# Performance work log

Measured on AMD Instinct MI355X. Metric: run time of the kernel, lower is better.

The kernel has to match this reference:

```python
import jax, jax.numpy as jnp
import numpy as np

B, HF, WF, C, A = 8, 32, 32, 1024, 9
N = B * HF * WF * A
IMG = 1024.0
K = 512                 # fixed candidate cap (replaces dynamic tf.where shape)
NUM_CLASSES = 80
FRCNN_FEAT = 256
ALIGN, SAMPLES = 7, 2
DET_THR, NMS_IOU = 0.7, 0.7
BN_EPS = 1e-3


def setup_inputs() -> dict:
    key = jax.random.key(0)
    ks = jax.random.split(key, 8)
    rpn_predictions = jax.random.normal(ks[0], (N,), jnp.float32)

    def rand_boxes(k):
        k1, k2, k3, k4 = jax.random.split(k, 4)
        cy = jax.random.uniform(k1, (N,), minval=0.0, maxval=IMG)
        cx = jax.random.uniform(k2, (N,), minval=0.0, maxval=IMG)
        h = jax.random.uniform(k3, (N,), minval=32.0, maxval=256.0)
        w = jax.random.uniform(k4, (N,), minval=32.0, maxval=256.0)
        return cy, cx, h, w

    cy, cx, h, w = rand_boxes(ks[1])
    rpn_anchors = jnp.stack([cy, cx, h, w], -1)  # center-point format [y,x,h,w]
    cy2, cx2, h2, w2 = rand_boxes(ks[2])
    rpn_rois = jnp.stack([
        jnp.clip(cy2 - h2 / 2, 0, IMG), jnp.clip(cx2 - w2 / 2, 0, IMG),
        jnp.clip(cy2 + h2 / 2, 0, IMG), jnp.clip(cx2 + w2 / 2, 0, IMG)], -1)
    rpn_assignments = jnp.repeat(jnp.arange(B, dtype=jnp.int32), HF * WF * A)
    images_features = jax.random.normal(ks[3], (B, HF, WF, C), jnp.float32)
    W1 = jax.random.normal(ks[4], (C, FRCNN_FEAT), jnp.float32) * 0.02
    b1 = jnp.zeros((FRCNN_FEAT,), jnp.float32)
    gamma = jnp.ones((FRCNN_FEAT,), jnp.float32)
    beta = jnp.zeros((FRCNN_FEAT,), jnp.float32)
    moving_mean = jnp.zeros((FRCNN_FEAT,), jnp.float32)
    moving_var = jnp.ones((FRCNN_FEAT,), jnp.float32)
    W2 = jax.random.normal(ks[5], (FRCNN_FEAT, 4 + NUM_CLASSES), jnp.float32) * 0.02
    b2 = jnp.zeros((4 + NUM_CLASSES,), jnp.float32)
    return dict(rpn_predictions=rpn_predictions, rpn_rois=rpn_rois,
                rpn_anchors=rpn_anchors, rpn_assignments=rpn_assignments,
                images_features=images_features, W1=W1, b1=b1, gamma=gamma,
                beta=beta, moving_mean=moving_mean, moving_var=moving_var,
                W2=W2, b2=b2)


def center_to_corners(a):
    y, x, h, w = a[:, 0], a[:, 1], a[:, 2], a[:, 3]
    return jnp.stack([y - h / 2, x - w / 2, y + h / 2, x + w / 2], -1)


def iou_one(box, boxes):
    yA = jnp.maximum(box[0], boxes[:, 0]); xA = jnp.maximum(box[1], boxes[:, 1])
    yB = jnp.minimum(box[2], boxes[:, 2]); xB = jnp.minimum(box[3], boxes[:, 3])
    inter = jnp.maximum(yB - yA, 0.0) * jnp.maximum(xB - xA, 0.0)
    a1 = (box[2] - box[0]) * (box[3] - box[1])
    a2 = (boxes[:, 2] - boxes[:, 0]) * (boxes[:, 3] - boxes[:, 1])
    return inter / (a1 + a2 - inter + 1e-8)


def greedy_nms(boxes, valid, thr):
    # boxes are already in score-descending order
    k = boxes.shape[0]
    idxs = jnp.arange(k)
    def body(i, keep):
        sup = (iou_one(boxes[i], boxes) > thr) & (idxs > i) & keep[i]
        return keep & ~sup
    return jax.lax.fori_loop(0, k, body, valid)


def roi_align_mean(feats, rois_n, assign):
    # feats [B,H,W,C]; rois_n [K,4] normalized corners; assign [K] batch idx
    Bf, H, W, Cf = feats.shape
    Kc = rois_n.shape[0]
    y1 = rois_n[:, 0] * H; x1 = rois_n[:, 1] * W
    y2 = rois_n[:, 2] * H; x2 = rois_n[:, 3] * W
    S = ALIGN * SAMPLES  # 14 samples per axis
    frac = (jnp.arange(S, dtype=feats.dtype) + 0.5) / S
    ys = y1[:, None] + frac * (y2 - y1)[:, None] - 0.5  # [K,S]
    xs = x1[:, None] + frac * (x2 - x1)[:, None] - 0.5
    yy = jnp.broadcast_to(ys[:, :, None], (Kc, S, S)).reshape(Kc, S * S)
    xx = jnp.broadcast_to(xs[:, None, :], (Kc, S, S)).reshape(Kc, S * S)
    yc = jnp.clip(yy, 0.0, H - 1.0); xc = jnp.clip(xx, 0.0, W - 1.0)
    y0 = jnp.floor(yc); x0 = jnp.floor(xc)
    wy = yc - y0; wx = xc - x0
    y0i = y0.astype(jnp.int32); x0i = x0.astype(jnp.int32)
    y1i = jnp.minimum(y0i + 1, H - 1); x1i = jnp.minimum(x0i + 1, W - 1)
    flat = feats.reshape(Bf * H * W, Cf)
    base = (assign.astype(jnp.int32) * H * W)[:, None]
    def g(yi, xi):
        return flat[(base + yi * W + xi).reshape(-1)].reshape(Kc, S * S, Cf)
    val = (((1 - wy) * (1 - wx))[..., None] * g(y0i, x0i)
           + ((1 - wy) * wx)[..., None] * g(y0i, x1i)
           + (wy * (1 - wx))[..., None] * g(y1i, x0i)
           + (wy * wx)[..., None] * g(y1i, x1i))
    # mean over all samples == mean over the 7x7 bins of per-bin sample means
    return val.mean(axis=1)  # [K,C]


def reference(rpn_predictions, rpn_rois, rpn_anchors, rpn_assignments,
              images_features, W1, b1, gamma, beta, moving_mean, moving_var,
              W2, b2):
    boxes_norm = jnp.array([IMG, IMG, IMG, IMG], jnp.float32)
    # --- threshold + gather (fixed-K top-k replaces dynamic tf.where) ---
    masked = jnp.where(rpn_predictions > DET_THR, rpn_predictions, -jnp.inf)
    top_scores, idx = jax.lax.top_k(masked, K)
    valid = jnp.isfinite(top_scores)
    rois = rpn_rois[idx]
    anchors = rpn_anchors[idx]
    assign = rpn_assignments[idx]
    # --- shift anchors per-image so NMS runs jointly across the batch ---
    shifted = center_to_corners(anchors) + assign[:, None].astype(jnp.float32) * boxes_norm
    # sigmoid is monotone -> score-descending order already holds
    keep = greedy_nms(shifted, valid, NMS_IOU)
    # --- ROI align + head (computed on all K, masked by keep) ---
    pooled = roi_align_mean(images_features, rois / boxes_norm, assign)  # [K,C]
    hdd = pooled @ W1 + b1
    hdd = (hdd - moving_mean) * jax.lax.rsqrt(moving_var + BN_EPS) * gamma + beta
    hdd = jax.nn.relu(hdd)  # dropout inactive at inference
    out = hdd @ W2 + b2  # [K, 4+num_classes]
    keepf = keep.astype(out.dtype)[:, None]
    frcnn_rois = (rois + out[:, :4]) * keepf
    frcnn_predictions = out[:, 4:] * keepf
    return frcnn_predictions, frcnn_rois, keep
```

## Files before the change

### kernel.cpp

```cpp
#include <hip/hip_runtime.h>
#include <stdint.h>

#define NTOT   73728
#define KSEL   512
#define DET_THRf 0.7f
#define NMS_THRf 0.7f
#define HFD    32
#define WFD    32
#define CCH    1024
#define IMGF   1024.0f
#define SAMP   14
#define FEAT1  256
#define OUTD   84
#define MAXC   4096
#define BUCKETS 256
#define BSCALE 48.0f
#define RB     4

#define WS_HIST     0
#define WS_CUTB     1024
#define WS_COUNTER  1028
#define WS_VALID    1032
#define WS_SELIDX   3080
#define WS_CSCORE   5136
#define WS_CIDX     21520
#define WS_ROIS     37904
#define WS_BOXES    46096
#define WS_ASSIGN   54288
#define WS_KEEPF    56336
#define WS_SUP      58384
#define WS_POOLED   91152

__device__ __forceinline__ int bucket_of(float s) {
  int b = (int)((s - DET_THRf) * BSCALE);
  return min(max(b, 0), BUCKETS - 1);
}

__global__ void k_hist(const float* __restrict__ pred, int* __restrict__ hist) {
  __shared__ int lh[BUCKETS];
  int t = threadIdx.x;
  lh[t] = 0;
  __syncthreads();
  for (int i = blockIdx.x * blockDim.x + t; i < NTOT; i += gridDim.x * blockDim.x) {
    float s = pred[i];
    if (s > DET_THRf) atomicAdd(&lh[bucket_of(s)], 1);
  }
  __syncthreads();
  if (lh[t]) atomicAdd(&hist[t], lh[t]);
}

__global__ void k_scan(const int* __restrict__ hist, int* __restrict__ cutB) {
  __shared__ int sh[BUCKETS];
  __shared__ int best;
  int t = threadIdx.x;
  sh[t] = hist[t];
  if (t == 0) best = -1;
  __syncthreads();
  for (int off = 1; off < BUCKETS; off <<= 1) {
    int v = sh[t] + ((t + off < BUCKETS) ? sh[t + off] : 0);
    __syncthreads();
    sh[t] = v;
    __syncthreads();
  }
  if (sh[t] >= KSEL) atomicMax(&best, t);
  __syncthreads();
  if (t == 0) *cutB = (best < 0) ? 0 : best;
}

__global__ void k_collect(const float* __restrict__ pred, const int* __restrict__ cutB,
                          int* __restrict__ counter, float* __restrict__ cs,
                          int* __restrict__ ci) {
  int B = *cutB;
  for (int i = blockIdx.x * blockDim.x + threadIdx.x; i < NTOT; i += gridDim.x * blockDim.x) {
    float s = pred[i];
    if (s > DET_THRf && bucket_of(s) >= B) {
      int p = atomicAdd(counter, 1);
      if (p < MAXC) { cs[p] = s; ci[p] = i; }
    }
  }
}

__global__ void __launch_bounds__(256) k_rank(
    const int* __restrict__ counter, const float* __restrict__ cs, const int* __restrict__ ci,
    int* __restrict__ sel_idx, int* __restrict__ valid) {
  __shared__ float s_s[MAXC];
  __shared__ int   s_i[MAXC];
  int t = threadIdx.x;
  int M = *counter; if (M > MAXC) M = MAXC;
  for (int j = t; j < M; j += 256) { s_s[j] = cs[j]; s_i[j] = ci[j]; }
  __syncthreads();
  int j = blockIdx.x * 256 + t;
  if (j >= M) return;
  float sj = s_s[j]; int ij = s_i[j];
  int r = 0;
  for (int m = 0; m < M; ++m) {
    float sm = s_s[m];
    r += (sm > sj) || (sm == sj && s_i[m] < ij);
  }
  if (r < KSEL) { sel_idx[r] = ij; valid[r] = 1; }
}

__global__ void k_gather(const int* __restrict__ sel_idx, const int* __restrict__ valid,
                         const float* __restrict__ rois, const float* __restrict__ anchors,
                         const int* __restrict__ assign,
                         int* __restrict__ assign_sel, float4* __restrict__ rois_sel,
                         float4* __restrict__ boxes_sh) {
  int t = threadIdx.x;
  if (t >= KSEL) return;
  int v = valid[t];
  int gi = v ? sel_idx[t] : 0;
  float4 rr = make_float4(0.f, 0.f, 0.f, 0.f);
  float4 bx = make_float4(0.f, 0.f, 0.f, 0.f);
  int aa = 0;
  if (v) {
    rr = make_float4(rois[gi*4+0], rois[gi*4+1], rois[gi*4+2], rois[gi*4+3]);
    float cy = anchors[gi*4+0], cx = anchors[gi*4+1];
    float h  = anchors[gi*4+2], w  = anchors[gi*4+3];
    aa = assign[gi];
    float off = (float)aa * IMGF;
    bx = make_float4(cy - h*0.5f + off, cx - w*0.5f + off,
                     cy + h*0.5f + off, cx + w*0.5f + off);
  }
  rois_sel[t] = rr;
  boxes_sh[t] = bx;
  assign_sel[t] = aa;
}

__global__ void k_ioumat(const float4* __restrict__ boxes,
                         unsigned long long* __restrict__ sup) {
  int wave = (blockIdx.x * blockDim.x + threadIdx.x) >> 6;
  int lane = threadIdx.x & 63;
  if (wave >= KSEL) return;
  float4 bi = boxes[wave];
  float a1 = (bi.z - bi.x) * (bi.w - bi.y);
  for (int c = 0; c < 8; ++c) {
    int col = c * 64 + lane;
    float4 bj = boxes[col];
    float yA = fmaxf(bi.x, bj.x), xA = fmaxf(bi.y, bj.y);
    float yB = fminf(bi.z, bj.z), xB = fminf(bi.w, bj.w);
    float inter = fmaxf(yB - yA, 0.f) * fmaxf(xB - xA, 0.f);
    float a2 = (bj.z - bj.x) * (bj.w - bj.y);
    float iou = inter / (a1 + a2 - inter + 1e-8f);
    bool s = (iou > NMS_THRf) && (col > wave);
    unsigned long long m = __ballot(s);
    if (lane == 0) sup[wave * 8 + c] = m;
  }
}

__global__ void k_sweep(const unsigned long long* __restrict__ sup,
                        const int* __restrict__ valid,
                        float* __restrict__ keep_ws, float* __restrict__ keep_out) {
  __shared__ unsigned char kb[KSEL];
  int t = threadIdx.x;
  for (int j = t; j < KSEL; j += 64) kb[j] = (unsigned char)valid[j];
  unsigned long long nz[8];
  for (int w = 0; w < 8; ++w) {
    int row = w * 64 + t;
    const unsigned long long* rp = &sup[row * 8];
    unsigned long long any = rp[0]|rp[1]|rp[2]|rp[3]|rp[4]|rp[5]|rp[6]|rp[7];
    nz[w] = __ballot(any != 0ull);
  }
  __syncthreads();
  if (t == 0) {
    for (int w = 0; w < 8; ++w) {
      unsigned long long bits = nz[w];
      while (bits) {
        int b = __ffsll((unsigned long long)bits) - 1;
        bits &= bits - 1;
        int i = w * 64 + b;
        if (kb[i]) {
          const unsigned long long* rp = &sup[i * 8];
          for (int c = 0; c < 8; ++c) {
            unsigned long long m = rp[c];
            while (m) {
              int bb = __ffsll((unsigned long long)m) - 1;
              m &= m - 1;
              kb[c * 64 + bb] = 0;
            }
          }
        }
      }
    }
  }
  __syncthreads();
  for (int j = t; j < KSEL; j += 64) {
    float kf = kb[j] ? 1.0f : 0.0f;
    keep_ws[j] = kf;
    keep_out[j] = kf;
  }
}

__global__ void __launch_bounds__(256) k_pool(
    const float* __restrict__ feats,
    const float4* __restrict__ rois_sel, const int* __restrict__ assign_sel,
    float* __restrict__ pooled) {
  int r = blockIdx.x;
  int t = threadIdx.x;

  __shared__ float Wy[HFD], Wx[WFD];
  __shared__ int bnds[4];
  __shared__ float wcomb[128];
  __shared__ int   ocomb[128];

  if (t < 32) { Wy[t] = 0.f; Wx[t] = 0.f; }
  __syncthreads();
  if (t == 0) {
    float4 roi = rois_sel[r];
    float sc = (float)HFD / IMGF;
    float y1 = roi.x * sc, x1 = roi.y * sc, y2 = roi.z * sc, x2 = roi.w * sc;
    int ymin = HFD - 1, ymax = 0, xmin = WFD - 1, xmax = 0;
    for (int s = 0; s < SAMP; ++s) {
      float fr = ((float)s + 0.5f) / (float)SAMP;
      float yc = y1 + fr * (y2 - y1) - 0.5f;
      yc = fminf(fmaxf(yc, 0.0f), (float)(HFD - 1));
      float y0f = floorf(yc);
      int y0 = (int)y0f;
      int y1i = min(y0 + 1, HFD - 1);
      float wy = yc - y0f;
      Wy[y0] += 1.0f - wy;
      Wy[y1i] += wy;
      ymin = min(ymin, y0); ymax = max(ymax, y1i);

      float xc = x1 + fr * (x2 - x1) - 0.5f;
      xc = fminf(fmaxf(xc, 0.0f), (float)(WFD - 1));
      float x0f = floorf(xc);
      int x0 = (int)x0f;
      int x1i = min(x0 + 1, WFD - 1);
      float wx = xc - x0f;
      Wx[x0] += 1.0f - wx;
      Wx[x1i] += wx;
      xmin = min(xmin, x0); xmax = max(xmax, x1i);
    }
    bnds[0] = ymin; bnds[1] = ymax; bnds[2] = xmin; bnds[3] = xmax;
  }
  __syncthreads();

  int ymin = bnds[0], xmin = bnds[2];
  int spanY = bnds[1] - ymin + 1;
  int spanX = bnds[3] - xmin + 1;
  int np = spanY * spanX;
  int b = assign_sel[r];
  const float inv = 1.0f / (float)(SAMP * SAMP);

  int ty = t >> 4, tx = t & 15;
  if (ty < spanY && tx < spanX) {
    int p = ty * spanX + tx;
    int y = ymin + ty, x = xmin + tx;
    wcomb[p] = Wy[y] * Wx[x] * inv;
    ocomb[p] = ((b * HFD + y) * WFD + x) * (CCH / 4);
  }
  __syncthreads();

  const float4* f4 = (const float4*)feats;
  float4 a0 = make_float4(0.f,0.f,0.f,0.f), a1 = a0, a2 = a0, a3 = a0;
  int p = 0;
  for (; p + 4 <= np; p += 4) {
    float w0 = wcomb[p],   w1 = wcomb[p+1], w2 = wcomb[p+2], w3 = wcomb[p+3];
    int   o0 = ocomb[p],   o1 = ocomb[p+1], o2 = ocomb[p+2], o3 = ocomb[p+3];
    float4 v0 = f4[o0 + t], v1 = f4[o1 + t], v2 = f4[o2 + t], v3 = f4[o3 + t];
    a0.x += w0*v0.x; a0.y += w0*v0.y; a0.z += w0*v0.z; a0.w += w0*v0.w;
    a1.x += w1*v1.x; a1.y += w1*v1.y; a1.z += w1*v1.z; a1.w += w1*v1.w;
    a2.x += w2*v2.x; a2.y += w2*v2.y; a2.z += w2*v2.z; a2.w += w2*v2.w;
    a3.x += w3*v3.x; a3.y += w3*v3.y; a3.z += w3*v3.z; a3.w += w3*v3.w;
  }
  for (; p < np; ++p) {
    float w = wcomb[p];
    float4 v = f4[ocomb[p] + t];
    a0.x += w*v.x; a0.y += w*v.y; a0.z += w*v.z; a0.w += w*v.w;
  }
  float4 s;
  s.x = (a0.x + a1.x) + (a2.x + a3.x);
  s.y = (a0.y + a1.y) + (a2.y + a3.y);
  s.z = (a0.z + a1.z) + (a2.z + a3.z);
  s.w = (a0.w + a1.w) + (a2.w + a3.w);
  ((float4*)pooled)[r * (CCH / 4) + t] = s;
}

__global__ void __launch_bounds__(256) k_fc(
    const float* __restrict__ pooled,
    const float* __restrict__ W1, const float* __restrict__ b1,
    const float* __restrict__ gamma, const float* __restrict__ beta,
    const float* __restrict__ mmean, const float* __restrict__ mvar,
    const float* __restrict__ W2, const float* __restrict__ b2,
    const float4* __restrict__ rois_sel, const float* __restrict__ keepf,
    float* __restrict__ pred_out, float* __restrict__ rois_out) {
  int r0 = blockIdx.x * RB;
  int t = threadIdx.x;
  __shared__ float hdd[RB][FEAT1];
  __shared__ float outv[RB][OUTD];

  const float* p0 = pooled + (r0 + 0) * CCH;
  const float* p1 = pooled + (r0 + 1) * CCH;
  const float* p2 = pooled + (r0 + 2) * CCH;
  const float* p3 = pooled + (r0 + 3) * CCH;

  float acc0 = 0.f, acc1 = 0.f, acc2 = 0.f, acc3 = 0.f;
  for (int c = 0; c < CCH; c += 4) {
    #pragma unroll
    for (int u = 0; u < 4; ++u) {
      float w = W1[(c + u) * FEAT1 + t];
      acc0 += p0[c + u] * w;
      acc1 += p1[c + u] * w;
      acc2 += p2[c + u] * w;
      acc3 += p3[c + u] * w;
    }
  }
  float bb = b1[t];
  float mn = mmean[t];
  float iv = rsqrtf(mvar[t] + 1e-3f) * gamma[t];
  float bt = beta[t];
  hdd[0][t] = fmaxf((acc0 + bb - mn) * iv + bt, 0.f);
  hdd[1][t] = fmaxf((acc1 + bb - mn) * iv + bt, 0.f);
  hdd[2][t] = fmaxf((acc2 + bb - mn) * iv + bt, 0.f);
  hdd[3][t] = fmaxf((acc3 + bb - mn) * iv + bt, 0.f);
  __syncthreads();

  for (int idx = t; idx < RB * OUTD; idx += 256) {
    int r = idx / OUTD, o = idx - OUTD * r;
    float s = b2[o];
    for (int k = 0; k < FEAT1; k += 4) {
      float4 h4 = *(const float4*)&hdd[r][k];
      s += h4.x * W2[(k+0) * OUTD + o];
      s += h4.y * W2[(k+1) * OUTD + o];
      s += h4.z * W2[(k+2) * OUTD + o];
      s += h4.w * W2[(k+3) * OUTD + o];
    }
    outv[r][o] = s;
  }
  __syncthreads();

  for (int idx = t; idx < RB * 80; idx += 256) {
    int r = idx / 80, j = idx - 80 * r;
    pred_out[(r0 + r) * 80 + j] = outv[r][4 + j] * keepf[r0 + r];
  }
  if (t < RB * 4) {
    int r = t >> 2, c = t & 3;
    float4 roi = rois_sel[r0 + r];
    float rc = (c == 0) ? roi.x : (c == 1) ? roi.y : (c == 2) ? roi.z : roi.w;
    rois_out[(r0 + r) * 4 + c] = (rc + outv[r][c]) * keepf[r0 + r];
  }
}

extern "C" void kernel_launch(void* const* d_in, const int* in_sizes, int n_in,
                              void* d_out, int out_size, void* d_ws, size_t ws_size,
                              hipStream_t stream) {
  const float* pred    = (const float*)d_in[0];
  const float* rois    = (const float*)d_in[1];
  const float* anchors = (const float*)d_in[2];
  const int*   assign  = (const int*)d_in[3];
  const float* feats   = (const float*)d_in[4];
  const float* W1      = (const float*)d_in[5];
  const float* b1      = (const float*)d_in[6];
  const float* gamma   = (const float*)d_in[7];
  const float* beta    = (const float*)d_in[8];
  const float* mmean   = (const float*)d_in[9];
  const float* mvar    = (const float*)d_in[10];
  const float* W2      = (const float*)d_in[11];
  const float* b2      = (const float*)d_in[12];

  char* ws = (char*)d_ws;
  int*   hist     = (int*)(ws + WS_HIST);
  int*   cutB     = (int*)(ws + WS_CUTB);
  int*   counter  = (int*)(ws + WS_COUNTER);
  int*   validp   = (int*)(ws + WS_VALID);
  int*   sel_idx  = (int*)(ws + WS_SELIDX);
  float* cscore   = (float*)(ws + WS_CSCORE);
  int*   cidx     = (int*)(ws + WS_CIDX);
  float4* rois_sel = (float4*)(ws + WS_ROIS);
  float4* boxes_sh = (float4*)(ws + WS_BOXES);
  int*   asel     = (int*)(ws + WS_ASSIGN);
  float* keepf    = (float*)(ws + WS_KEEPF);
  unsigned long long* sup = (unsigned long long*)(ws + WS_SUP);
  float* pooled   = (float*)(ws + WS_POOLED);

  float* pred_out = (float*)d_out;
  float* rois_out = pred_out + KSEL * 80;
  float* keep_out = rois_out + KSEL * 4;

  hipMemsetAsync(ws, 0, 3080, stream);

  k_hist<<<64, BUCKETS, 0, stream>>>(pred, hist);
  k_scan<<<1, BUCKETS, 0, stream>>>(hist, cutB);
  k_collect<<<64, 256, 0, stream>>>(pred, cutB, counter, cscore, cidx);
  k_rank<<<MAXC / 256, 256, 0, stream>>>(counter, cscore, cidx, sel_idx, validp);
  k_gather<<<1, KSEL, 0, stream>>>(sel_idx, validp, rois, anchors, assign,
                                   asel, rois_sel, boxes_sh);
  k_ioumat<<<128, 256, 0, stream>>>(boxes_sh, sup);
  k_sweep<<<1, 64, 0, stream>>>(sup, validp, keepf, keep_out);
  k_pool<<<KSEL, 256, 0, stream>>>(feats, rois_sel, asel, pooled);
  k_fc<<<KSEL / RB, 256, 0, stream>>>(pooled, W1, b1, gamma, beta, mmean, mvar,
                                      W2, b2, rois_sel, keepf,
                                      pred_out, rois_out);
}
```

Before: 212.9 us.

## Fuse pipeline into fewer kernels with last-block reductions and split-K FC

Merges histogram+scan, collect+rank, gather+pool and ioumat+sweep into single kernels, using a last-block-done atomic counter so the follow-up serial step runs inside the same launch. The first FC layer is split along K into four partial GEMMs over 8-row tiles, with a separate kernel that sums the partials and runs BN, ReLU and the second layer. Pool unrolls to 8 independent loads. The goal is fewer launches and more parallel FC work. In exchange, the ranking now runs on a single block and partial sums add a workspace round trip.

```diff
diff --git a/kernel.cpp b/kernel.cpp
--- a/kernel.cpp
+++ b/kernel.cpp
@@ -15,197 +15,128 @@
 #define MAXC   4096
 #define BUCKETS 256
 #define BSCALE 48.0f
-#define RB     4
+#define KSPLIT 4
+#define FRB    8
 
 #define WS_HIST     0
 #define WS_CUTB     1024
 #define WS_COUNTER  1028
-#define WS_VALID    1032
-#define WS_SELIDX   3080
-#define WS_CSCORE   5136
-#define WS_CIDX     21520
-#define WS_ROIS     37904
-#define WS_BOXES    46096
-#define WS_ASSIGN   54288
-#define WS_KEEPF    56336
-#define WS_SUP      58384
-#define WS_POOLED   91152
+#define WS_DONE0    1032
+#define WS_DONE1    1036
+#define WS_DONE2    1040
+#define WS_VALID    1056
+#define WS_SELIDX   3104
+#define WS_CSCORE   5152
+#define WS_CIDX     21536
+#define WS_ROIS     37920
+#define WS_KEEPF    46112
+#define WS_SUP      48160
+#define WS_POOLED   80928
+#define WS_PART     2178080
 
 __device__ __forceinline__ int bucket_of(float s) {
   int b = (int)((s - DET_THRf) * BSCALE);
   return min(max(b, 0), BUCKETS - 1);
 }
 
-__global__ void k_hist(const float* __restrict__ pred, int* __restrict__ hist) {
+__global__ void __launch_bounds__(256) k_topsel1(const float* __restrict__ pred,
+                                                 int* __restrict__ hist,
+                                                 int* __restrict__ done,
+                                                 int* __restrict__ cutB) {
   __shared__ int lh[BUCKETS];
+  __shared__ int lastf;
+  __shared__ int best;
   int t = threadIdx.x;
   lh[t] = 0;
   __syncthreads();
-  for (int i = blockIdx.x * blockDim.x + t; i < NTOT; i += gridDim.x * blockDim.x) {
+  for (int i = blockIdx.x * 256 + t; i < NTOT; i += gridDim.x * 256) {
     float s = pred[i];
     if (s > DET_THRf) atomicAdd(&lh[bucket_of(s)], 1);
   }
   __syncthreads();
-  if (lh[t]) atomicAdd(&hist[t], lh[t]);
-}
-
-__global__ void k_scan(const int* __restrict__ hist, int* __restrict__ cutB) {
-  __shared__ int sh[BUCKETS];
-  __shared__ int best;
+  atomicAdd(&hist[t], lh[t]);
+  __threadfence();
+  __syncthreads();
+  if (t == 0) lastf = (atomicAdd(done, 1) == (int)gridDim.x - 1);
+  __syncthreads();
+  if (!lastf) return;
+  __threadfence();
+  int h = atomicAdd(&hist[t], 0);
+  lh[t] = h;
+  if (t == 0) best = 0;
+  __syncthreads();
+  for (int off = 1; off < BUCKETS; off <<= 1) {
+    int v = lh[t] + ((t + off < BUCKETS) ? lh[t + off] : 0);
+    __syncthreads();
+    lh[t] = v;
+    __syncthreads();
+  }
+  if (lh[t] >= KSEL) atomicMax(&best, t);
+  __syncthreads();
+  if (t == 0) *cutB = best;
+}
+
+__global__ void __launch_bounds__(256) k_topsel2(const float* __restrict__ pred,
+                                                 const int* __restrict__ cutB,
+                                                 int* __restrict__ counter,
+                                                 float* __restrict__ cs, int* __restrict__ ci,
+                                                 int* __restrict__ done,
+                                                 int* __restrict__ sel_idx, int* __restrict__ valid) {
+  __shared__ int lastf;
   int t = threadIdx.x;
-  sh[t] = hist[t];
-  if (t == 0) best = -1;
-  __syncthreads();
-  for (int off = 1; off < BUCKETS; off <<= 1) {
-    int v = sh[t] + ((t + off < BUCKETS) ? sh[t + off] : 0);
-    __syncthreads();
-    sh[t] = v;
-    __syncthreads();
-  }
-  if (sh[t] >= KSEL) atomicMax(&best, t);
-  __syncthreads();
-  if (t == 0) *cutB = (best < 0) ? 0 : best;
-}
-
-__global__ void k_collect(const float* __restrict__ pred, const int* __restrict__ cutB,
-                          int* __restrict__ counter, float* __restrict__ cs,
-                          int* __restrict__ ci) {
   int B = *cutB;
-  for (int i = blockIdx.x * blockDim.x + threadIdx.x; i < NTOT; i += gridDim.x * blockDim.x) {
+  for (int i = blockIdx.x * 256 + t; i < NTOT; i += gridDim.x * 256) {
     float s = pred[i];
     if (s > DET_THRf && bucket_of(s) >= B) {
       int p = atomicAdd(counter, 1);
       if (p < MAXC) { cs[p] = s; ci[p] = i; }
     }
   }
-}
-
-__global__ void __launch_bounds__(256) k_rank(
-    const int* __restrict__ counter, const float* __restrict__ cs, const int* __restrict__ ci,
-    int* __restrict__ sel_idx, int* __restrict__ valid) {
+  __threadfence();
+  __syncthreads();
+  if (t == 0) lastf = (atomicAdd(done, 1) == (int)gridDim.x - 1);
+  __syncthreads();
+  if (!lastf) return;
+  __threadfence();
   __shared__ float s_s[MAXC];
   __shared__ int   s_i[MAXC];
-  int t = threadIdx.x;
-  int M = *counter; if (M > MAXC) M = MAXC;
+  int M = atomicAdd(counter, 0);
+  if (M > MAXC) M = MAXC;
   for (int j = t; j < M; j += 256) { s_s[j] = cs[j]; s_i[j] = ci[j]; }
   __syncthreads();
-  int j = blockIdx.x * 256 + t;
-  if (j >= M) return;
-  float sj = s_s[j]; int ij = s_i[j];
-  int r = 0;
-  for (int m = 0; m < M; ++m) {
-    float sm = s_s[m];
-    r += (sm > sj) || (sm == sj && s_i[m] < ij);
-  }
-  if (r < KSEL) { sel_idx[r] = ij; valid[r] = 1; }
-}
-
-__global__ void k_gather(const int* __restrict__ sel_idx, const int* __restrict__ valid,
-                         const float* __restrict__ rois, const float* __restrict__ anchors,
-                         const int* __restrict__ assign,
-                         int* __restrict__ assign_sel, float4* __restrict__ rois_sel,
-                         float4* __restrict__ boxes_sh) {
-  int t = threadIdx.x;
-  if (t >= KSEL) return;
-  int v = valid[t];
-  int gi = v ? sel_idx[t] : 0;
-  float4 rr = make_float4(0.f, 0.f, 0.f, 0.f);
-  float4 bx = make_float4(0.f, 0.f, 0.f, 0.f);
-  int aa = 0;
-  if (v) {
-    rr = make_float4(rois[gi*4+0], rois[gi*4+1], rois[gi*4+2], rois[gi*4+3]);
-    float cy = anchors[gi*4+0], cx = anchors[gi*4+1];
-    float h  = anchors[gi*4+2], w  = anchors[gi*4+3];
-    aa = assign[gi];
-    float off = (float)aa * IMGF;
-    bx = make_float4(cy - h*0.5f + off, cx - w*0.5f + off,
-                     cy + h*0.5f + off, cx + w*0.5f + off);
-  }
-  rois_sel[t] = rr;
-  boxes_sh[t] = bx;
-  assign_sel[t] = aa;
-}
-
-__global__ void k_ioumat(const float4* __restrict__ boxes,
-                         unsigned long long* __restrict__ sup) {
-  int wave = (blockIdx.x * blockDim.x + threadIdx.x) >> 6;
-  int lane = threadIdx.x & 63;
-  if (wave >= KSEL) return;
-  float4 bi = boxes[wave];
-  float a1 = (bi.z - bi.x) * (bi.w - bi.y);
-  for (int c = 0; c < 8; ++c) {
-    int col = c * 64 + lane;
-    float4 bj = boxes[col];
-    float yA = fmaxf(bi.x, bj.x), xA = fmaxf(bi.y, bj.y);
-    float yB = fminf(bi.z, bj.z), xB = fminf(bi.w, bj.w);
-    float inter = fmaxf(yB - yA, 0.f) * fmaxf(xB - xA, 0.f);
-    float a2 = (bj.z - bj.x) * (bj.w - bj.y);
-    float iou = inter / (a1 + a2 - inter + 1e-8f);
-    bool s = (iou > NMS_THRf) && (col > wave);
-    unsigned long long m = __ballot(s);
-    if (lane == 0) sup[wave * 8 + c] = m;
-  }
-}
-
-__global__ void k_sweep(const unsigned long long* __restrict__ sup,
-                        const int* __restrict__ valid,
-                        float* __restrict__ keep_ws, float* __restrict__ keep_out) {
-  __shared__ unsigned char kb[KSEL];
-  int t = threadIdx.x;
-  for (int j = t; j < KSEL; j += 64) kb[j] = (unsigned char)valid[j];
-  unsigned long long nz[8];
-  for (int w = 0; w < 8; ++w) {
-    int row = w * 64 + t;
-    const unsigned long long* rp = &sup[row * 8];
-    unsigned long long any = rp[0]|rp[1]|rp[2]|rp[3]|rp[4]|rp[5]|rp[6]|rp[7];
-    nz[w] = __ballot(any != 0ull);
-  }
+  for (int j = t; j < M; j += 256) {
+    float sj = s_s[j]; int ij = s_i[j];
+    int r = 0;
+    for (int m = 0; m < M; ++m) {
+      float sm = s_s[m];
+      r += (sm > sj) || (sm == sj && s_i[m] < ij);
+    }
+    if (r < KSEL) { sel_idx[r] = ij; valid[r] = 1; }
+  }
+}
+
+__global__ void __launch_bounds__(256) k_pool(const float* __restrict__ feats,
+                                              const float* __restrict__ rois,
+                                              const int* __restrict__ assign,
+                                              const int* __restrict__ sel_idx,
+                                              const int* __restrict__ valid,
+                                              float* __restrict__ pooled,
+                                              float4* __restrict__ rois_sel) {
+  int r = blockIdx.x, t = threadIdx.x;
+  __shared__ float Wy[HFD], Wx[WFD];
+  __shared__ int bnds[5];
+  __shared__ float wcomb[160];
+  __shared__ int   ocomb[160];
+
+  if (t < 32) { Wy[t] = 0.f; Wx[t] = 0.f; }
   __syncthreads();
   if (t == 0) {
-    for (int w = 0; w < 8; ++w) {
-      unsigned long long bits = nz[w];
-      while (bits) {
-        int b = __ffsll((unsigned long long)bits) - 1;
-        bits &= bits - 1;
-        int i = w * 64 + b;
-        if (kb[i]) {
-          const unsigned long long* rp = &sup[i * 8];
-          for (int c = 0; c < 8; ++c) {
-            unsigned long long m = rp[c];
-            while (m) {
-              int bb = __ffsll((unsigned long long)m) - 1;
-              m &= m - 1;
-              kb[c * 64 + bb] = 0;
-            }
-          }
-        }
-      }
-    }
-  }
-  __syncthreads();
-  for (int j = t; j < KSEL; j += 64) {
-    float kf = kb[j] ? 1.0f : 0.0f;
-    keep_ws[j] = kf;
-    keep_out[j] = kf;
-  }
-}
-
-__global__ void __launch_bounds__(256) k_pool(
-    const float* __restrict__ feats,
-    const float4* __restrict__ rois_sel, const int* __restrict__ assign_sel,
-    float* __restrict__ pooled) {
-  int r = blockIdx.x;
-  int t = threadIdx.x;
-
-  __shared__ float Wy[HFD], Wx[WFD];
-  __shared__ int bnds[4];
-  __shared__ float wcomb[128];
-  __shared__ int   ocomb[128];
-
-  if (t < 32) { Wy[t] = 0.f; Wx[t] = 0.f; }
-  __syncthreads();
-  if (t == 0) {
-    float4 roi = rois_sel[r];
+    int v = valid[r];
+    int gi = v ? sel_idx[r] : 0;
+    float4 roi = make_float4(0.f, 0.f, 0.f, 0.f);
+    int b = 0;
+    if (v) { roi = *(const float4*)&rois[gi * 4]; b = assign[gi]; }
+    rois_sel[r] = roi;
     float sc = (float)HFD / IMGF;
     float y1 = roi.x * sc, x1 = roi.y * sc, y2 = roi.z * sc, x2 = roi.w * sc;
     int ymin = HFD - 1, ymax = 0, xmin = WFD - 1, xmax = 0;
@@ -231,7 +162,7 @@
       Wx[x1i] += wx;
       xmin = min(xmin, x0); xmax = max(xmax, x1i);
     }
-    bnds[0] = ymin; bnds[1] = ymax; bnds[2] = xmin; bnds[3] = xmax;
+    bnds[0] = ymin; bnds[1] = ymax; bnds[2] = xmin; bnds[3] = xmax; bnds[4] = b;
   }
   __syncthreads();
 
@@ -239,101 +170,210 @@
   int spanY = bnds[1] - ymin + 1;
   int spanX = bnds[3] - xmin + 1;
   int np = spanY * spanX;
-  int b = assign_sel[r];
+  int b = bnds[4];
   const float inv = 1.0f / (float)(SAMP * SAMP);
-
-  int ty = t >> 4, tx = t & 15;
-  if (ty < spanY && tx < spanX) {
-    int p = ty * spanX + tx;
-    int y = ymin + ty, x = xmin + tx;
+  for (int p = t; p < np; p += 256) {
+    int py = p / spanX, px = p - py * spanX;
+    int y = ymin + py, x = xmin + px;
     wcomb[p] = Wy[y] * Wx[x] * inv;
     ocomb[p] = ((b * HFD + y) * WFD + x) * (CCH / 4);
   }
   __syncthreads();
 
   const float4* f4 = (const float4*)feats;
-  float4 a0 = make_float4(0.f,0.f,0.f,0.f), a1 = a0, a2 = a0, a3 = a0;
+  float4 a[8];
+  #pragma unroll
+  for (int j = 0; j < 8; ++j) a[j] = make_float4(0.f, 0.f, 0.f, 0.f);
   int p = 0;
-  for (; p + 4 <= np; p += 4) {
-    float w0 = wcomb[p],   w1 = wcomb[p+1], w2 = wcomb[p+2], w3 = wcomb[p+3];
-    int   o0 = ocomb[p],   o1 = ocomb[p+1], o2 = ocomb[p+2], o3 = ocomb[p+3];
-    float4 v0 = f4[o0 + t], v1 = f4[o1 + t], v2 = f4[o2 + t], v3 = f4[o3 + t];
-    a0.x += w0*v0.x; a0.y += w0*v0.y; a0.z += w0*v0.z; a0.w += w0*v0.w;
-    a1.x += w1*v1.x; a1.y += w1*v1.y; a1.z += w1*v1.z; a1.w += w1*v1.w;
-    a2.x += w2*v2.x; a2.y += w2*v2.y; a2.z += w2*v2.z; a2.w += w2*v2.w;
-    a3.x += w3*v3.x; a3.y += w3*v3.y; a3.z += w3*v3.z; a3.w += w3*v3.w;
+  for (; p + 8 <= np; p += 8) {
+    float w[8]; int o[8]; float4 v[8];
+    #pragma unroll
+    for (int j = 0; j < 8; ++j) { w[j] = wcomb[p + j]; o[j] = ocomb[p + j]; }
+    #pragma unroll
+    for (int j = 0; j < 8; ++j) v[j] = f4[o[j] + t];
+    #pragma unroll
+    for (int j = 0; j < 8; ++j) {
+      a[j].x += w[j] * v[j].x; a[j].y += w[j] * v[j].y;
+      a[j].z += w[j] * v[j].z; a[j].w += w[j] * v[j].w;
+    }
   }
   for (; p < np; ++p) {
     float w = wcomb[p];
     float4 v = f4[ocomb[p] + t];
-    a0.x += w*v.x; a0.y += w*v.y; a0.z += w*v.z; a0.w += w*v.w;
-  }
-  float4 s;
-  s.x = (a0.x + a1.x) + (a2.x + a3.x);
-  s.y = (a0.y + a1.y) + (a2.y + a3.y);
-  s.z = (a0.z + a1.z) + (a2.z + a3.z);
-  s.w = (a0.w + a1.w) + (a2.w + a3.w);
-  ((float4*)pooled)[r * (CCH / 4) + t] = s;
-}
-
-__global__ void __launch_bounds__(256) k_fc(
-    const float* __restrict__ pooled,
-    const float* __restrict__ W1, const float* __restrict__ b1,
-    const float* __restrict__ gamma, const float* __restrict__ beta,
-    const float* __restrict__ mmean, const float* __restrict__ mvar,
-    const float* __restrict__ W2, const float* __restrict__ b2,
-    const float4* __restrict__ rois_sel, const float* __restrict__ keepf,
-    float* __restrict__ pred_out, float* __restrict__ rois_out) {
-  int r0 = blockIdx.x * RB;
+    a[0].x += w * v.x; a[0].y += w * v.y; a[0].z += w * v.z; a[0].w += w * v.w;
+  }
+  #pragma unroll
+  for (int j = 1; j < 8; ++j) {
+    a[0].x += a[j].x; a[0].y += a[j].y; a[0].z += a[j].z; a[0].w += a[j].w;
+  }
+  ((float4*)pooled)[r * (CCH / 4) + t] = a[0];
+}
+
+__global__ void __launch_bounds__(256) k_fc1(const float* __restrict__ pooled,
+                                             const float* __restrict__ W1,
+                                             float* __restrict__ part) {
+  int r0 = blockIdx.x * FRB;
+  int kb = blockIdx.y;
   int t = threadIdx.x;
-  __shared__ float hdd[RB][FEAT1];
-  __shared__ float outv[RB][OUTD];
-
-  const float* p0 = pooled + (r0 + 0) * CCH;
-  const float* p1 = pooled + (r0 + 1) * CCH;
-  const float* p2 = pooled + (r0 + 2) * CCH;
-  const float* p3 = pooled + (r0 + 3) * CCH;
-
-  float acc0 = 0.f, acc1 = 0.f, acc2 = 0.f, acc3 = 0.f;
-  for (int c = 0; c < CCH; c += 4) {
+  __shared__ float sp[FRB][256];
+  for (int idx = t; idx < FRB * 256; idx += 256) {
+    int r = idx >> 8, c = idx & 255;
+    sp[r][c] = pooled[(r0 + r) * CCH + kb * 256 + c];
+  }
+  __syncthreads();
+  int lane = t & 63, wv = t >> 6;
+  int o4 = lane * 4;
+  float4 acc[FRB];
+  #pragma unroll
+  for (int r = 0; r < FRB; ++r) acc[r] = make_float4(0.f, 0.f, 0.f, 0.f);
+  const float* Wbase = W1 + (kb * 256 + wv * 64) * FEAT1 + o4;
+  int kwb = wv * 64;
+  #pragma unroll 4
+  for (int c = 0; c < 64; ++c) {
+    float4 w4 = *(const float4*)(Wbase + c * FEAT1);
+    int kk = kwb + c;
     #pragma unroll
-    for (int u = 0; u < 4; ++u) {
-      float w = W1[(c + u) * FEAT1 + t];
-      acc0 += p0[c + u] * w;
-      acc1 += p1[c + u] * w;
-      acc2 += p2[c + u] * w;
-      acc3 += p3[c + u] * w;
-    }
-  }
-  float bb = b1[t];
-  float mn = mmean[t];
+    for (int r = 0; r < FRB; ++r) {
+      float pv = sp[r][kk];
+      acc[r].x += pv * w4.x; acc[r].y += pv * w4.y;
+      acc[r].z += pv * w4.z; acc[r].w += pv * w4.w;
+    }
+  }
+  #pragma unroll
+  for (int r = 0; r < FRB; ++r)
+    *(float4*)&part[((kb * KSEL) + (r0 + r)) * FEAT1 + o4] = acc[r];
+}
+
+__global__ void __launch_bounds__(512) k_nms(const int* __restrict__ sel_idx,
+                                             const int* __restrict__ valid,
+                                             const float* __restrict__ anchors,
+                                             const int* __restrict__ assign,
+                                             unsigned long long* __restrict__ sup,
+                                             int* __restrict__ done,
+                                             float* __restrict__ keepf,
+                                             float* __restrict__ keep_out) {
+  __shared__ float4 boxes[KSEL];
+  __shared__ unsigned char kb[KSEL];
+  __shared__ unsigned long long nzsh[8];
+  __shared__ int lastf;
+  int t = threadIdx.x;
+  {
+    int v = valid[t];
+    int gi = v ? sel_idx[t] : 0;
+    float4 bx = make_float4(0.f, 0.f, 0.f, 0.f);
+    if (v) {
+      float4 an = *(const float4*)&anchors[gi * 4];
+      float off = (float)assign[gi] * IMGF;
+      bx = make_float4(an.x - an.z * 0.5f + off, an.y - an.w * 0.5f + off,
+                       an.x + an.z * 0.5f + off, an.y + an.w * 0.5f + off);
+    }
+    boxes[t] = bx;
+  }
+  __syncthreads();
+  int wave = t >> 6, lane = t & 63;
+  int row = blockIdx.x * 8 + wave;
+  float4 bi = boxes[row];
+  float a1 = (bi.z - bi.x) * (bi.w - bi.y);
+  for (int c = 0; c < 8; ++c) {
+    int col = c * 64 + lane;
+    float4 bj = boxes[col];
+    float yA = fmaxf(bi.x, bj.x), xA = fmaxf(bi.y, bj.y);
+    float yB = fminf(bi.z, bj.z), xB = fminf(bi.w, bj.w);
+    float inter = fmaxf(yB - yA, 0.f) * fmaxf(xB - xA, 0.f);
+    float a2 = (bj.z - bj.x) * (bj.w - bj.y);
+    float iou = inter / (a1 + a2 - inter + 1e-8f);
+    bool s = (iou > NMS_THRf) && (col > row);
+    unsigned long long m = __ballot(s);
+    if (lane == 0) sup[row * 8 + c] = m;
+  }
+  __threadfence();
+  __syncthreads();
+  if (t == 0) lastf = (atomicAdd(done, 1) == (int)gridDim.x - 1);
+  __syncthreads();
+  if (!lastf) return;
+  __threadfence();
+  kb[t] = (unsigned char)valid[t];
+  if (t < 64) {
+    for (int w = 0; w < 8; ++w) {
+      const unsigned long long* rp = &sup[(w * 64 + t) * 8];
+      unsigned long long any = rp[0]|rp[1]|rp[2]|rp[3]|rp[4]|rp[5]|rp[6]|rp[7];
+      unsigned long long m = __ballot(any != 0ull);
+      if (t == 0) nzsh[w] = m;
+    }
+  }
+  __syncthreads();
+  if (t == 0) {
+    for (int w = 0; w < 8; ++w) {
+      unsigned long long bits = nzsh[w];
+      while (bits) {
+        int b = __ffsll((unsigned long long)bits) - 1;
+        bits &= bits - 1;
+        int i = w * 64 + b;
+        if (kb[i]) {
+          const unsigned long long* rp = &sup[i * 8];
+          for (int c2 = 0; c2 < 8; ++c2) {
+            unsigned long long m = rp[c2];
+            while (m) {
+              int bb = __ffsll((unsigned long long)m) - 1;
+              m &= m - 1;
+              kb[c2 * 64 + bb] = 0;
+            }
+          }
+        }
+      }
+    }
+  }
+  __syncthreads();
+  {
+    float kf = kb[t] ? 1.0f : 0.0f;
+    keepf[t] = kf;
+    keep_out[t] = kf;
+  }
+}
+
+__global__ void __launch_bounds__(256) k_fc2(const float* __restrict__ part,
+                                             const float* __restrict__ b1,
+                                             const float* __restrict__ gamma,
+                                             const float* __restrict__ beta,
+                                             const float* __restrict__ mmean,
+                                             const float* __restrict__ mvar,
+                                             const float* __restrict__ W2,
+                                             const float* __restrict__ b2,
+                                             const float4* __restrict__ rois_sel,
+                                             const float* __restrict__ keepf,
+                                             float* __restrict__ pred_out,
+                                             float* __restrict__ rois_out) {
+  int r0 = blockIdx.x * FRB;
+  int t = threadIdx.x;
+  __shared__ float hdd[FRB][FEAT1];
+  __shared__ float outv[FRB][OUTD];
+
+  float bb = b1[t], mn = mmean[t];
   float iv = rsqrtf(mvar[t] + 1e-3f) * gamma[t];
   float bt = beta[t];
-  hdd[0][t] = fmaxf((acc0 + bb - mn) * iv + bt, 0.f);
-  hdd[1][t] = fmaxf((acc1 + bb - mn) * iv + bt, 0.f);
-  hdd[2][t] = fmaxf((acc2 + bb - mn) * iv + bt, 0.f);
-  hdd[3][t] = fmaxf((acc3 + bb - mn) * iv + bt, 0.f);
-  __syncthreads();
-
-  for (int idx = t; idx < RB * OUTD; idx += 256) {
+  #pragma unroll
+  for (int r = 0; r < FRB; ++r) {
+    int ri = r0 + r;
+    float s = part[(0 * KSEL + ri) * FEAT1 + t] + part[(1 * KSEL + ri) * FEAT1 + t]
+            + part[(2 * KSEL + ri) * FEAT1 + t] + part[(3 * KSEL + ri) * FEAT1 + t];
+    hdd[r][t] = fmaxf((s + bb - mn) * iv + bt, 0.f);
+  }
+  __syncthreads();
+
+  for (int idx = t; idx < FRB * OUTD; idx += 256) {
     int r = idx / OUTD, o = idx - OUTD * r;
     float s = b2[o];
-    for (int k = 0; k < FEAT1; k += 4) {
-      float4 h4 = *(const float4*)&hdd[r][k];
-      s += h4.x * W2[(k+0) * OUTD + o];
-      s += h4.y * W2[(k+1) * OUTD + o];
-      s += h4.z * W2[(k+2) * OUTD + o];
-      s += h4.w * W2[(k+3) * OUTD + o];
-    }
+    #pragma unroll 4
+    for (int k = 0; k < FEAT1; ++k) s += hdd[r][k] * W2[k * OUTD + o];
     outv[r][o] = s;
   }
   __syncthreads();
 
-  for (int idx = t; idx < RB * 80; idx += 256) {
+  for (int idx = t; idx < FRB * 80; idx += 256) {
     int r = idx / 80, j = idx - 80 * r;
     pred_out[(r0 + r) * 80 + j] = outv[r][4 + j] * keepf[r0 + r];
   }
-  if (t < RB * 4) {
+  if (t < FRB * 4) {
     int r = t >> 2, c = t & 3;
     float4 roi = rois_sel[r0 + r];
     float rc = (c == 0) ? roi.x : (c == 1) ? roi.y : (c == 2) ? roi.z : roi.w;
@@ -362,33 +402,34 @@
   int*   hist     = (int*)(ws + WS_HIST);
   int*   cutB     = (int*)(ws + WS_CUTB);
   int*   counter  = (int*)(ws + WS_COUNTER);
+  int*   done0    = (int*)(ws + WS_DONE0);
+  int*   done1    = (int*)(ws + WS_DONE1);
+  int*   done2    = (int*)(ws + WS_DONE2);
   int*   validp   = (int*)(ws + WS_VALID);
   int*   sel_idx  = (int*)(ws + WS_SELIDX);
   float* cscore   = (float*)(ws + WS_CSCORE);
   int*   cidx     = (int*)(ws + WS_CIDX);
   float4* rois_sel = (float4*)(ws + WS_ROIS);
-  float4* boxes_sh = (float4*)(ws + WS_BOXES);
-  int*   asel     = (int*)(ws + WS_ASSIGN);
   float* keepf    = (float*)(ws + WS_KEEPF);
   unsigned long long* sup = (unsigned long long*)(ws + WS_SUP);
   float* pooled   = (float*)(ws + WS_POOLED);
+  float* part     = (float*)(ws + WS_PART);
 
   float* pred_out = (float*)d_out;
   float* rois_out = pred_out + KSEL * 80;
   float* keep_out = rois_out + KSEL * 4;
 
-  hipMemsetAsync(ws, 0, 3080, stream);
-
-  k_hist<<<64, BUCKETS, 0, stream>>>(pred, hist);
-  k_scan<<<1, BUCKETS, 0, stream>>>(hist, cutB);
-  k_collect<<<64, 256, 0, stream>>>(pred, cutB, counter, cscore, cidx);
-  k_rank<<<MAXC / 256, 256, 0, stream>>>(counter, cscore, cidx, sel_idx, validp);
-  k_gather<<<1, KSEL, 0, stream>>>(sel_idx, validp, rois, anchors, assign,
-                                   asel, rois_sel, boxes_sh);
-  k_ioumat<<<128, 256, 0, stream>>>(boxes_sh, sup);
-  k_sweep<<<1, 64, 0, stream>>>(sup, validp, keepf, keep_out);
-  k_pool<<<KSEL, 256, 0, stream>>>(feats, rois_sel, asel, pooled);
-  k_fc<<<KSEL / RB, 256, 0, stream>>>(pooled, W1, b1, gamma, beta, mmean, mvar,
-                                      W2, b2, rois_sel, keepf,
-                                      pred_out, rois_out);
-}
+  hipMemsetAsync(ws, 0, 5152, stream);
+
+  k_topsel1<<<64, 256, 0, stream>>>(pred, hist, done0, cutB);
+  k_topsel2<<<64, 256, 0, stream>>>(pred, cutB, counter, cscore, cidx, done1,
+                                    sel_idx, validp);
+  k_pool<<<KSEL, 256, 0, stream>>>(feats, rois, assign, sel_idx, validp,
+                                   pooled, rois_sel);
+  k_fc1<<<dim3(KSEL / FRB, KSPLIT), 256, 0, stream>>>(pooled, W1, part);
+  k_nms<<<64, 512, 0, stream>>>(sel_idx, validp, anchors, assign, sup, done2,
+                                keepf, keep_out);
+  k_fc2<<<KSEL / FRB, 256, 0, stream>>>(part, b1, gamma, beta, mmean, mvar,
+                                        W2, b2, rois_sel, keepf,
+                                        pred_out, rois_out);
+}
```

New measurement: 243.2 us. 14.2% more time.
